# Kernel tuning notes

Measured on AMD Instinct MI355X. Metric: run time of the kernel, lower is better.

Reference implementation:

```python
import jax, jax.numpy as jnp
import numpy as np

# 3D multi-scale deformable attention (MSDeformAttn, n_heads=8 / 3D variant)
LEVEL_SHAPES = [(32, 32, 32), (16, 16, 16), (8, 8, 8), (4, 4, 4)]  # (H, W, D) per level
D_MODEL, N_HEADS, N_LEVELS, N_POINTS = 256, 8, 4, 4
C_HEAD = D_MODEL // N_HEADS  # 32
N_BATCH, LEN_Q = 1, 37440
LEN_IN = sum(h * w * d for h, w, d in LEVEL_SHAPES)  # 37440


def setup_inputs() -> dict:
    key = jax.random.key(0)
    ks = jax.random.split(key, 10)
    s = 0.02  # param init scale
    return {
        "query": jax.random.normal(ks[0], (N_BATCH, LEN_Q, D_MODEL), jnp.float32),
        "reference_points": jax.random.uniform(ks[1], (N_BATCH, LEN_Q, N_LEVELS, 3), jnp.float32),
        "input_flatten": jax.random.normal(ks[2], (N_BATCH, LEN_IN, D_MODEL), jnp.float32),
        "input_spatial_shapes": jnp.array(LEVEL_SHAPES, dtype=jnp.int32),
        "input_level_start_index": jnp.array(
            np.cumsum([0] + [h * w * d for h, w, d in LEVEL_SHAPES])[:-1], dtype=jnp.int32),
        "W_value": s * jax.random.normal(ks[3], (D_MODEL, D_MODEL), jnp.float32),
        "b_value": jnp.zeros((D_MODEL,), jnp.float32),
        "W_off": s * jax.random.normal(ks[4], (D_MODEL, N_HEADS * N_LEVELS * N_POINTS * 3), jnp.float32),
        "b_off": s * jax.random.normal(ks[5], (N_HEADS * N_LEVELS * N_POINTS * 3,), jnp.float32),
        "W_attn": s * jax.random.normal(ks[6], (D_MODEL, N_HEADS * N_LEVELS * N_POINTS), jnp.float32),
        "b_attn": jnp.zeros((N_HEADS * N_LEVELS * N_POINTS,), jnp.float32),
        "W_out": s * jax.random.normal(ks[7], (D_MODEL, D_MODEL), jnp.float32),
        "b_out": jnp.zeros((D_MODEL,), jnp.float32),
    }


def trilinear_sample(vol, gx, gy, gz):
    """torch F.grid_sample 3D, mode=bilinear, padding=zeros, align_corners=False.
    vol: (B, C, Dz, Dy, Dx); gx indexes Dx, gy indexes Dy, gz indexes Dz, each (B, Q) in [-1,1].
    Returns (B, C, Q)."""
    B, C, Dz, Dy, Dx = vol.shape
    ix = ((gx + 1.0) * Dx - 1.0) * 0.5
    iy = ((gy + 1.0) * Dy - 1.0) * 0.5
    iz = ((gz + 1.0) * Dz - 1.0) * 0.5
    x0f, y0f, z0f = jnp.floor(ix), jnp.floor(iy), jnp.floor(iz)
    fx, fy, fz = ix - x0f, iy - y0f, iz - z0f
    x0, y0, z0 = x0f.astype(jnp.int32), y0f.astype(jnp.int32), z0f.astype(jnp.int32)
    vol_f = vol.reshape(B, C, Dz * Dy * Dx)
    out = jnp.zeros((B, C, gx.shape[1]), vol.dtype)
    for dz in (0, 1):
        for dy in (0, 1):
            for dx in (0, 1):
                xc, yc, zc = x0 + dx, y0 + dy, z0 + dz
                w = ((fx if dx else 1.0 - fx) * (fy if dy else 1.0 - fy) * (fz if dz else 1.0 - fz))
                valid = ((xc >= 0) & (xc < Dx) & (yc >= 0) & (yc < Dy) & (zc >= 0) & (zc < Dz))
                idx = (jnp.clip(zc, 0, Dz - 1) * Dy + jnp.clip(yc, 0, Dy - 1)) * Dx + jnp.clip(xc, 0, Dx - 1)
                v = jnp.take_along_axis(vol_f, idx[:, None, :], axis=2)  # (B, C, Q)
                out = out + (w * valid.astype(w.dtype))[:, None, :] * v
    return out


def reference(query, reference_points, input_flatten, input_spatial_shapes,
              input_level_start_index, W_value, b_value, W_off, b_off,
              W_attn, b_attn, W_out, b_out):
    N, Lq, _ = query.shape
    Lin = input_flatten.shape[1]
    value = (input_flatten @ W_value + b_value).reshape(N, Lin, N_HEADS, C_HEAD)
    off = (query @ W_off + b_off).reshape(N, Lq, N_HEADS, N_LEVELS, N_POINTS, 3)
    attn = jax.nn.softmax((query @ W_attn + b_attn).reshape(N, Lq, N_HEADS, N_LEVELS * N_POINTS), axis=-1)
    # offset_normalizer = [W, H, D] per level (as in the torch code)
    norm = jnp.stack([input_spatial_shapes[:, 1], input_spatial_shapes[:, 0],
                      input_spatial_shapes[:, 2]], -1).astype(query.dtype)
    loc = reference_points[:, :, None, :, None, :] + off / norm[None, None, None, :, None, :]
    grids = 2.0 * loc - 1.0  # (N, Lq, M, L, P, 3)
    starts = np.cumsum([0] + [h * w * d for h, w, d in LEVEL_SHAPES])
    sampled = []
    for l, (H, W, D) in enumerate(LEVEL_SHAPES):
        vl = value[:, starts[l]:starts[l + 1]]  # (N, H*W*D, M, C)
        vol = (vl.reshape(N, H, W, D, N_HEADS, C_HEAD)
                 .transpose(0, 4, 5, 1, 2, 3)
                 .reshape(N * N_HEADS, C_HEAD, H, W, D))
        g = grids[:, :, :, l].transpose(0, 2, 1, 3, 4).reshape(N * N_HEADS, Lq * N_POINTS, 3)
        # grid x indexes last vol dim (D), y indexes W, z indexes H (torch grid_sample convention)
        s = trilinear_sample(vol, g[..., 0], g[..., 1], g[..., 2])  # (N*M, C, Lq*P)
        sampled.append(s.reshape(N * N_HEADS, C_HEAD, Lq, N_POINTS))
    samp = jnp.stack(sampled, axis=-2).reshape(N * N_HEADS, C_HEAD, Lq, N_LEVELS * N_POINTS)
    aw = attn.transpose(0, 2, 1, 3).reshape(N * N_HEADS, 1, Lq, N_LEVELS * N_POINTS)
    out = (samp * aw).sum(-1).reshape(N, N_HEADS * C_HEAD, Lq).transpose(0, 2, 1)
    return out @ W_out + b_out
```

## Files before the change

### kernel.cpp

```cpp
#include <hip/hip_runtime.h>
#include <math.h>

#define LQ      37440
#define LIN     37440
#define DMODEL  256
#define NHEADS  8
#define CHEAD   32
#define K_DIM   256

#define VALB_DELTA (LIN * 256 + 32)

typedef __attribute__((ext_vector_type(8))) short short8;
typedef __attribute__((ext_vector_type(4))) short short4v;
typedef __attribute__((ext_vector_type(4))) float f32x4;
typedef __attribute__((ext_vector_type(2))) float f32x2;

__device__ inline unsigned short bf16_rte(float f) {
    union { float f; unsigned u; } v; v.f = f;
    return (unsigned short)((v.u + 0x7fffu + ((v.u >> 16) & 1u)) >> 16);
}
__device__ inline float bf16_f(unsigned short s) {
    union { unsigned u; float f; } v; v.u = ((unsigned)s) << 16;
    return v.f;
}
__device__ inline float bits_f(unsigned u) {
    union { unsigned u; float f; } v; v.u = u;
    return v.f;
}
__device__ inline unsigned pkbf(float a, float b) {
    return (unsigned)bf16_rte(a) | ((unsigned)bf16_rte(b) << 16);
}

__device__ __forceinline__ void gl_lds16(const unsigned short* g, unsigned short* l) {
    __builtin_amdgcn_global_load_lds(
        (const __attribute__((address_space(1))) void*)g,
        (__attribute__((address_space(3))) void*)l, 16, 0, 0);
}

__global__ __launch_bounds__(256) void prep_all(
        const float* __restrict__ inp, const float* __restrict__ query,
        const float* __restrict__ Wv, const float* __restrict__ Wo,
        const float* __restrict__ Wa, const float* __restrict__ Wout,
        const float* __restrict__ bo, const float* __restrict__ ba,
        unsigned short* __restrict__ in_b, unsigned short* __restrict__ q_b,
        unsigned short* __restrict__ Bv, unsigned short* __restrict__ Bq,
        unsigned short* __restrict__ Bw, float* __restrict__ bias_m,
        unsigned short* __restrict__ padA,
        unsigned short* __restrict__ valB,
        int n4)
{
    const int bid = blockIdx.x;
    if (bid < 9360) {
        int i = bid * 256 + threadIdx.x;
        int j = i * 2;
        const float* src;
        unsigned short* dst;
        int jj;
        if (j < n4) { src = inp;   dst = in_b; jj = j; }
        else        { src = query; dst = q_b;  jj = j - n4; }
        float4 v0 = ((const float4*)src)[jj];
        float4 v1 = ((const float4*)src)[jj + 1];
        int4 o;
        o.x = (int)pkbf(v0.x, v0.y);
        o.y = (int)pkbf(v0.z, v0.w);
        o.z = (int)pkbf(v1.x, v1.y);
        o.w = (int)pkbf(v1.z, v1.w);
        ((int4*)dst)[jj >> 1] = o;
    } else {
        int i = (bid - 9360) * 256 + threadIdx.x;
        int n = i >> 8, k = i & 255;
        if (n < 256) {
            Bv[(size_t)n * 256 + k] = bf16_rte(Wv[(size_t)k * 256 + n]);
        } else if (n < 640) {
            int m = n - 256;
            Bq[(size_t)m * 256 + k] = bf16_rte(Wo[(size_t)k * 384 + m]);
        } else if (n < 768) {
            int m = n - 640;
            Bq[(size_t)(384 + m) * 256 + k] = bf16_rte(Wa[(size_t)k * 128 + m]);
        } else {
            int m = n - 768;
            Bw[(size_t)m * 256 + k] = bf16_rte(Wout[(size_t)k * 256 + m]);
        }
        if (i < 512) bias_m[i] = (i < 384) ? bo[i] : ba[i - 384];
        if (i < 64)       padA[i] = 0;
        else if (i < 96)  valB[i - 64] = 0;
        else if (i < 192) valB[(size_t)LIN * 256 + 32 + (i - 96)] = 0;
    }
}

__global__ __launch_bounds__(256) void gemm2(
    const unsigned short* __restrict__ in_b, const unsigned short* __restrict__ q_b,
    const unsigned short* __restrict__ Bv,   const unsigned short* __restrict__ Bq,
    const float* __restrict__ bv, const float* __restrict__ bias_m,
    unsigned short* __restrict__ value_t, unsigned short* __restrict__ valB,
    unsigned short* __restrict__ qbuf)
{
    __shared__ __align__(16) unsigned short SH[16384];
    unsigned short* AsL = SH;
    unsigned short* BsL = SH + 8192;

    const int t    = threadIdx.x;
    const int bm   = blockIdx.y * 128;
    const int w    = t >> 6;
    const int lane = t & 63;
    const int lm   = lane & 15;
    const int quad = lane >> 4;

    const int isval = (blockIdx.x < 2);
    const unsigned short* A  = isval ? in_b : q_b;
    const unsigned short* Bt = isval ? Bv : Bq;
    const float* bias        = isval ? bv : bias_m;
    const int n0             = (isval ? blockIdx.x : (blockIdx.x - 2)) * 128;

    const unsigned short* ga[2]; const unsigned short* gb[2];
    int loff[2];
    #pragma unroll
    for (int i = 0; i < 2; ++i) {
        int idx = i * 256 + t;
        int row = idx >> 2;
        int chn = (idx & 3) ^ ((row >> 1) & 3);
        int rga = bm + row; if (rga >= LQ) rga = LQ - 1;
        ga[i] = A  + (size_t)rga * K_DIM + chn * 8;
        gb[i] = Bt + (size_t)(n0 + row) * K_DIM + chn * 8;
        loff[i] = i * 2048 + w * 512;
    }

    const int ra0 = w * 32 + lm, ra1 = ra0 + 16;
    const int aoff0 = ra0 * 32 + ((quad ^ ((ra0 >> 1) & 3)) << 3);
    const int aoff1 = ra1 * 32 + ((quad ^ ((ra1 >> 1) & 3)) << 3);
    int boff[8];
    #pragma unroll
    for (int nt = 0; nt < 8; ++nt) {
        int rb = nt * 16 + lm;
        boff[nt] = rb * 32 + ((quad ^ ((rb >> 1) & 3)) << 3);
    }

    f32x4 acc[2][8];
    #pragma unroll
    for (int mt = 0; mt < 2; ++mt)
        #pragma unroll
        for (int nt = 0; nt < 8; ++nt)
            acc[mt][nt] = (f32x4){0.f, 0.f, 0.f, 0.f};

    #define STAGE(K0, SEL) do { \
        gl_lds16(ga[0] + (K0), AsL + (SEL) * 4096 + loff[0]); \
        gl_lds16(ga[1] + (K0), AsL + (SEL) * 4096 + loff[1]); \
        gl_lds16(gb[0] + (K0), BsL + (SEL) * 4096 + loff[0]); \
        gl_lds16(gb[1] + (K0), BsL + (SEL) * 4096 + loff[1]); \
    } while (0)

    STAGE(0, 0);
    #pragma unroll
    for (int kt = 0; kt < 8; ++kt) {
        const int sel = kt & 1;
        if (kt < 7) {
            STAGE((kt + 1) * 32, sel ^ 1);
            asm volatile("s_waitcnt vmcnt(4)" ::: "memory");
        } else {
            asm volatile("s_waitcnt vmcnt(0)" ::: "memory");
        }
        __builtin_amdgcn_s_barrier();

        const int so = sel * 4096;
        short8 af[2], bf[8];
        af[0] = *(const short8*)&AsL[so + aoff0];
        af[1] = *(const short8*)&AsL[so + aoff1];
        #pragma unroll
        for (int nt = 0; nt < 8; ++nt)
            bf[nt] = *(const short8*)&BsL[so + boff[nt]];
        #pragma unroll
        for (int mt = 0; mt < 2; ++mt)
            #pragma unroll
            for (int nt = 0; nt < 8; ++nt)
                acc[mt][nt] = __builtin_amdgcn_mfma_f32_16x16x32_bf16(af[mt], bf[nt], acc[mt][nt], 0, 0, 0);

        asm volatile("s_waitcnt lgkmcnt(0)" ::: "memory");
        __builtin_amdgcn_s_barrier();
    }
    #undef STAGE

    unsigned short* SHc = SH;
    #pragma unroll
    for (int nt = 0; nt < 8; ++nt) {
        int col = nt * 16 + lm;
        float bb = bias[n0 + col];
        #pragma unroll
        for (int mt = 0; mt < 2; ++mt) {
            int rb = w * 32 + mt * 16 + quad * 4;
            #pragma unroll
            for (int r = 0; r < 4; ++r)
                SHc[(rb + r) * 128 + col] = bf16_rte(acc[mt][nt][r] + bb);
        }
    }
    __syncthreads();

    if (isval) {
        const int h0 = n0 >> 5;
        #pragma unroll
        for (int k = 0; k < 8; ++k) {
            int ci  = t + k * 256;
            int hl  = ci >> 9;
            int rem = ci & 511;
            int row = rem >> 2;
            int cq  = (rem & 3) << 3;
            int4 v = *(const int4*)&SHc[row * 128 + hl * 32 + cq];
            int grow = bm + row;
            if (grow < LQ) {
                size_t e = ((size_t)(h0 + hl) * LIN + grow) * 32 + cq;
                *(int4*)&value_t[e] = v;
                *(int4*)&valB[32 + e] = v;
            }
        }
    } else {
        #pragma unroll
        for (int k = 0; k < 8; ++k) {
            int ci  = t + k * 256;
            int row = ci >> 4;
            int cq  = (ci & 15) << 3;
            int4 v = *(const int4*)&SHc[row * 128 + cq];
            int grow = bm + row;
            if (grow < LQ)
                *(int4*)&qbuf[(size_t)grow * 512 + n0 + cq] = v;
        }
    }
}

__global__ __launch_bounds__(256) void gemm_out(
    const unsigned short* __restrict__ A, const unsigned short* __restrict__ Bt,
    const float* __restrict__ bias, float* __restrict__ Cout)
{
    __shared__ __align__(16) unsigned short SH[16384];
    unsigned short* AsL = SH;
    unsigned short* BsL = SH + 8192;

    const int t    = threadIdx.x;
    const int bm   = blockIdx.y * 128;
    const int n0   = blockIdx.x * 128;
    const int w    = t >> 6;
    const int lane = t & 63;
    const int lm   = lane & 15;
    const int quad = lane >> 4;

    const unsigned short* ga[2]; const unsigned short* gb[2];
    int loff[2];
    #pragma unroll
    for (int i = 0; i < 2; ++i) {
        int idx = i * 256 + t;
        int row = idx >> 2;
        int chn = (idx & 3) ^ ((row >> 1) & 3);
        int rga = bm + row; if (rga >= LQ) rga = LQ - 1;
        ga[i] = A  + (size_t)rga * K_DIM + chn * 8;
        gb[i] = Bt + (size_t)(n0 + row) * K_DIM + chn * 8;
        loff[i] = i * 2048 + w * 512;
    }

    const int ra0 = w * 32 + lm, ra1 = ra0 + 16;
    const int aoff0 = ra0 * 32 + ((quad ^ ((ra0 >> 1) & 3)) << 3);
    const int aoff1 = ra1 * 32 + ((quad ^ ((ra1 >> 1) & 3)) << 3);
    int boff[8];
    #pragma unroll
    for (int nt = 0; nt < 8; ++nt) {
        int rb = nt * 16 + lm;
        boff[nt] = rb * 32 + ((quad ^ ((rb >> 1) & 3)) << 3);
    }

    f32x4 acc[2][8];
    #pragma unroll
    for (int mt = 0; mt < 2; ++mt)
        #pragma unroll
        for (int nt = 0; nt < 8; ++nt)
            acc[mt][nt] = (f32x4){0.f, 0.f, 0.f, 0.f};

    #define STAGE(K0, SEL) do { \
        gl_lds16(ga[0] + (K0), AsL + (SEL) * 4096 + loff[0]); \
        gl_lds16(ga[1] + (K0), AsL + (SEL) * 4096 + loff[1]); \
        gl_lds16(gb[0] + (K0), BsL + (SEL) * 4096 + loff[0]); \
        gl_lds16(gb[1] + (K0), BsL + (SEL) * 4096 + loff[1]); \
    } while (0)

    STAGE(0, 0);
    #pragma unroll
    for (int kt = 0; kt < 8; ++kt) {
        const int sel = kt & 1;
        if (kt < 7) {
            STAGE((kt + 1) * 32, sel ^ 1);
            asm volatile("s_waitcnt vmcnt(4)" ::: "memory");
        } else {
            asm volatile("s_waitcnt vmcnt(0)" ::: "memory");
        }
        __builtin_amdgcn_s_barrier();

        const int so = sel * 4096;
        short8 af[2], bf[8];
        af[0] = *(const short8*)&AsL[so + aoff0];
        af[1] = *(const short8*)&AsL[so + aoff1];
        #pragma unroll
        for (int nt = 0; nt < 8; ++nt)
            bf[nt] = *(const short8*)&BsL[so + boff[nt]];
        #pragma unroll
        for (int mt = 0; mt < 2; ++mt)
            #pragma unroll
            for (int nt = 0; nt < 8; ++nt)
                acc[mt][nt] = __builtin_amdgcn_mfma_f32_16x16x32_bf16(af[mt], bf[nt], acc[mt][nt], 0, 0, 0);

        asm volatile("s_waitcnt lgkmcnt(0)" ::: "memory");
        __builtin_amdgcn_s_barrier();
    }
    #undef STAGE

    float* SHf = (float*)SH;
    #pragma unroll
    for (int p = 0; p < 2; ++p) {
        if (p) __syncthreads();
        #pragma unroll
        for (int nt = 0; nt < 8; ++nt) {
            int col = nt * 16 + lm;
            float bb = bias[n0 + col];
            int lrow = w * 16 + quad * 4;
            #pragma unroll
            for (int r = 0; r < 4; ++r)
                SHf[(lrow + r) * 128 + col] = acc[p][nt][r] + bb;
        }
        __syncthreads();
        #pragma unroll
        for (int k = 0; k < 8; ++k) {
            int ci  = t + k * 256;
            int lr  = ci >> 5;
            int cq  = (ci & 31) << 2;
            int4 v = *(const int4*)&SHf[lr * 128 + cq];
            int grow = bm + (lr >> 4) * 32 + p * 16 + (lr & 15);
            if (grow < LQ)
                *(int4*)&Cout[(size_t)grow * 256 + n0 + cq] = v;
        }
    }
}

__global__ __launch_bounds__(256) void sample_kernel(
    const float* __restrict__ refp,
    const unsigned short* __restrict__ qbuf,
    const unsigned short* __restrict__ value_t,
    unsigned short* __restrict__ samp)
{
    __shared__ float4 zywS[4][16][8];
    __shared__ f32x2  wxS [4][16][8];
    __shared__ int4   ozyS[4][16][8];

    const int t  = threadIdx.x;
    const int q0 = blockIdx.x * 4;

    const int   Sz[4]   = {32, 16, 8, 4};
    const float invS[4] = {1.f/32.f, 1.f/16.f, 1.f/8.f, 1.f/4.f};
    const int   St[4]   = {0, 32768, 36864, 37376};

    #pragma unroll
    for (int pi = t; pi < 512; pi += 256) {
        int ql = pi >> 7;
        int hp = pi & 127;
        int hh = hp >> 4;
        int c  = hp & 15;
        int l  = c >> 2;
        int q  = q0 + ql;
        const unsigned short* o = qbuf + (size_t)q * 512 + hp * 3;
        const float* r = refp + q * 12 + l * 3;
        const int   S  = Sz[l];
        const float Sf = (float)S;
        const float is = invS[l];
        float ix = (r[0] + bf16_f(o[0]) * is) * Sf - 0.5f;
        float iy = (r[1] + bf16_f(o[1]) * is) * Sf - 0.5f;
        float iz = (r[2] + bf16_f(o[2]) * is) * Sf - 0.5f;
        float xf = floorf(ix), yf = floorf(iy), zf = floorf(iz);
        float fx = ix - xf, fy = iy - yf, fz = iz - zf;
        int x0 = (int)xf, y0 = (int)yf, z0 = (int)zf;

        float wx0 = (x0 >= 0  && x0 < S)     ? (1.f - fx) : 0.f;
        float wx1 = (x0 >= -1 && x0 < S - 1) ? fx         : 0.f;
        float wy0 = (y0 >= 0  && y0 < S)     ? (1.f - fy) : 0.f;
        float wy1 = (y0 >= -1 && y0 < S - 1) ? fy         : 0.f;
        float wz0 = (z0 >= 0  && z0 < S)     ? (1.f - fz) : 0.f;
        float wz1 = (z0 >= -1 && z0 < S - 1) ? fz         : 0.f;

        int cy0 = min(max(y0, 0), S - 1), cy1 = min(max(y0 + 1, 0), S - 1);
        int cz0 = min(max(z0, 0), S - 1), cz1 = min(max(z0 + 1, 0), S - 1);

        float lgv = bf16_f(qbuf[(size_t)q * 512 + 384 + hp]);
        float m = fmaxf(lgv, __shfl_xor(lgv, 1));
        m = fmaxf(m, __shfl_xor(m, 2));
        m = fmaxf(m, __shfl_xor(m, 4));
        m = fmaxf(m, __shfl_xor(m, 8));
        float e = __expf(lgv - m);
        float s = e + __shfl_xor(e, 1);
        s += __shfl_xor(s, 2);
        s += __shfl_xor(s, 4);
        s += __shfl_xor(s, 8);
        float a = __fdividef(e, s);

        const int S2 = S * S;
        const int st = St[l];
        const int xb = x0 * 32 + ((x0 & 1) ? VALB_DELTA : 0);
        zywS[ql][c][hh] = make_float4(wz0*wy0, wz0*wy1, wz1*wy0, wz1*wy1);
        wxS [ql][c][hh] = (f32x2){wx0 * a, wx1 * a};
        ozyS[ql][c][hh] = make_int4((st + cz0*S2 + cy0*S) * 32 + xb,
                                    (st + cz0*S2 + cy1*S) * 32 + xb,
                                    (st + cz1*S2 + cy0*S) * 32 + xb,
                                    (st + cz1*S2 + cy1*S) * 32 + xb);
    }
    __syncthreads();

    const int ql   = t >> 6;
    const int lane = t & 63;
    const int hh   = lane >> 3;
    const int j    = lane & 7;
    const int xsel = j >> 2;
    const int cgrp = (j & 3) << 3;
    const int q    = q0 + ql;

    const unsigned short* vbase = value_t - 64;
    const unsigned laneoff = (unsigned)(hh * (LIN * 32) + j * 8 + 64);

    f32x2 acc0 = {0.f,0.f}, acc1 = {0.f,0.f}, acc2 = {0.f,0.f}, acc3 = {0.f,0.f};

    #pragma unroll
    for (int c = 0; c < 16; ++c) {
        float4 zyw = zywS[ql][c][hh];
        f32x2  wx  = wxS [ql][c][hh];
        int4   zo  = ozyS[ql][c][hh];
        float  ws  = xsel ? wx.y : wx.x;

        #define CORNER(OFF, WZ) { \
            int4 v = *(const int4*)(vbase + (laneoff + (unsigned)(OFF))); \
            float w_ = (WZ) * ws; \
            f32x2 w2 = {w_, w_}; \
            acc0 += w2 * (f32x2){bits_f(((unsigned)v.x) << 16), bits_f((unsigned)v.x)}; \
            acc1 += w2 * (f32x2){bits_f(((unsigned)v.y) << 16), bits_f((unsigned)v.y)}; \
            acc2 += w2 * (f32x2){bits_f(((unsigned)v.z) << 16), bits_f((unsigned)v.z)}; \
            acc3 += w2 * (f32x2){bits_f(((unsigned)v.w) << 16), bits_f((unsigned)v.w)}; }

        CORNER(zo.x, zyw.x);
        CORNER(zo.y, zyw.y);
        CORNER(zo.z, zyw.z);
        CORNER(zo.w, zyw.w);
        #undef CORNER
    }

    float c0 = acc0.x + __shfl_xor(acc0.x, 4);
    float c1 = acc0.y + __shfl_xor(acc0.y, 4);
    float c2 = acc1.x + __shfl_xor(acc1.x, 4);
    float c3 = acc1.y + __shfl_xor(acc1.y, 4);
    float c4 = acc2.x + __shfl_xor(acc2.x, 4);
    float c5 = acc2.y + __shfl_xor(acc2.y, 4);
    float c6 = acc3.x + __shfl_xor(acc3.x, 4);
    float c7 = acc3.y + __shfl_xor(acc3.y, 4);
    if (xsel == 0) {
        int4 o = make_int4((int)pkbf(c0, c1), (int)pkbf(c2, c3),
                           (int)pkbf(c4, c5), (int)pkbf(c6, c7));
        *(int4*)(samp + (size_t)q * DMODEL + hh * CHEAD + cgrp) = o;
    }
}

extern "C" void kernel_launch(void* const* d_in, const int* in_sizes, int n_in,
                              void* d_out, int out_size, void* d_ws, size_t ws_size,
                              hipStream_t stream) {
    const float* query = (const float*)d_in[0];
    const float* refp  = (const float*)d_in[1];
    const float* inp   = (const float*)d_in[2];
    const float* Wv   = (const float*)d_in[5];
    const float* bv   = (const float*)d_in[6];
    const float* Wo   = (const float*)d_in[7];
    const float* bo   = (const float*)d_in[8];
    const float* Wa   = (const float*)d_in[9];
    const float* ba   = (const float*)d_in[10];
    const float* Wout = (const float*)d_in[11];
    const float* bout = (const float*)d_in[12];

    char* p = (char*)d_ws;
    p += 256;
    unsigned short* value_t = (unsigned short*)p; p += (size_t)LIN * 256 * 2;
    unsigned short* valB    = (unsigned short*)p; p += ((size_t)LIN * 256 + 128) * 2;
    unsigned short* qbuf    = (unsigned short*)p; p += (size_t)LQ * 512 * 2;
    unsigned short* samp    = (unsigned short*)p; p += (size_t)LQ * 256 * 2;
    unsigned short* in_b    = (unsigned short*)p; p += (size_t)LQ * 256 * 2;
    unsigned short* q_b     = (unsigned short*)p; p += (size_t)LQ * 256 * 2;
    unsigned short* Bv   = (unsigned short*)p;    p += 256 * 256 * 2;
    unsigned short* Bq   = (unsigned short*)p;    p += 512 * 256 * 2;
    unsigned short* Bw   = (unsigned short*)p;    p += 256 * 256 * 2;
    float* bias_m = (float*)p;                    p += 512 * 4;

    const int n4 = LQ * 256 / 4;
    dim3 blk(256);

    prep_all<<<9360 + 1024, blk, 0, stream>>>(
        inp, query, Wv, Wo, Wa, Wout, bo, ba,
        in_b, q_b, Bv, Bq, Bw, bias_m, value_t - 64, valB, n4);
    gemm2<<<dim3(6, (LQ + 127) / 128), blk, 0, stream>>>(
        in_b, q_b, Bv, Bq, bv, bias_m, value_t, valB, qbuf);
    sample_kernel<<<LQ / 4, blk, 0, stream>>>(refp, qbuf, value_t, samp);
    gemm_out<<<dim3(2, (LQ + 127) / 128), blk, 0, stream>>>(samp, Bw, bout, (float*)d_out);
}
```

Measured before the change: 295.1 us.

## Fuse fp32-to-bf16 activation conversion into GEMM and remap blocks per XCD

The separate conversion pass that turned input and query into bf16 buffers is removed. The GEMM now loads the fp32 A rows directly, converts them in registers and writes them into the swizzled LDS tile, overlapping that work with the MFMA loop. This saves one full write and re-read of two 37440x256 activation tensors. Both GEMMs also remap block IDs so that consecutive tiles stay on the same XCD for L2 locality, and the sampling kernel is split into two half-range launches. The trade-offs are twice the A-operand global bytes inside the GEMM, a full vmcnt(0) wait each iteration instead of the earlier partial wait, and one extra kernel launch.

```diff
diff --git a/kernel.cpp b/kernel.cpp
--- a/kernel.cpp
+++ b/kernel.cpp
@@ -37,59 +37,37 @@
         (__attribute__((address_space(3))) void*)l, 16, 0, 0);
 }
 
-__global__ __launch_bounds__(256) void prep_all(
-        const float* __restrict__ inp, const float* __restrict__ query,
+__global__ __launch_bounds__(256) void prep_w(
         const float* __restrict__ Wv, const float* __restrict__ Wo,
         const float* __restrict__ Wa, const float* __restrict__ Wout,
         const float* __restrict__ bo, const float* __restrict__ ba,
-        unsigned short* __restrict__ in_b, unsigned short* __restrict__ q_b,
         unsigned short* __restrict__ Bv, unsigned short* __restrict__ Bq,
         unsigned short* __restrict__ Bw, float* __restrict__ bias_m,
         unsigned short* __restrict__ padA,
-        unsigned short* __restrict__ valB,
-        int n4)
+        unsigned short* __restrict__ valB)
 {
-    const int bid = blockIdx.x;
-    if (bid < 9360) {
-        int i = bid * 256 + threadIdx.x;
-        int j = i * 2;
-        const float* src;
-        unsigned short* dst;
-        int jj;
-        if (j < n4) { src = inp;   dst = in_b; jj = j; }
-        else        { src = query; dst = q_b;  jj = j - n4; }
-        float4 v0 = ((const float4*)src)[jj];
-        float4 v1 = ((const float4*)src)[jj + 1];
-        int4 o;
-        o.x = (int)pkbf(v0.x, v0.y);
-        o.y = (int)pkbf(v0.z, v0.w);
-        o.z = (int)pkbf(v1.x, v1.y);
-        o.w = (int)pkbf(v1.z, v1.w);
-        ((int4*)dst)[jj >> 1] = o;
+    int i = blockIdx.x * 256 + threadIdx.x;
+    int n = i >> 8, k = i & 255;
+    if (n < 256) {
+        Bv[(size_t)n * 256 + k] = bf16_rte(Wv[(size_t)k * 256 + n]);
+    } else if (n < 640) {
+        int m = n - 256;
+        Bq[(size_t)m * 256 + k] = bf16_rte(Wo[(size_t)k * 384 + m]);
+    } else if (n < 768) {
+        int m = n - 640;
+        Bq[(size_t)(384 + m) * 256 + k] = bf16_rte(Wa[(size_t)k * 128 + m]);
     } else {
-        int i = (bid - 9360) * 256 + threadIdx.x;
-        int n = i >> 8, k = i & 255;
-        if (n < 256) {
-            Bv[(size_t)n * 256 + k] = bf16_rte(Wv[(size_t)k * 256 + n]);
-        } else if (n < 640) {
-            int m = n - 256;
-            Bq[(size_t)m * 256 + k] = bf16_rte(Wo[(size_t)k * 384 + m]);
-        } else if (n < 768) {
-            int m = n - 640;
-            Bq[(size_t)(384 + m) * 256 + k] = bf16_rte(Wa[(size_t)k * 128 + m]);
-        } else {
-            int m = n - 768;
-            Bw[(size_t)m * 256 + k] = bf16_rte(Wout[(size_t)k * 256 + m]);
-        }
-        if (i < 512) bias_m[i] = (i < 384) ? bo[i] : ba[i - 384];
-        if (i < 64)       padA[i] = 0;
-        else if (i < 96)  valB[i - 64] = 0;
-        else if (i < 192) valB[(size_t)LIN * 256 + 32 + (i - 96)] = 0;
-    }
+        int m = n - 768;
+        Bw[(size_t)m * 256 + k] = bf16_rte(Wout[(size_t)k * 256 + m]);
+    }
+    if (i < 512) bias_m[i] = (i < 384) ? bo[i] : ba[i - 384];
+    if (i < 64)       padA[i] = 0;
+    else if (i < 96)  valB[i - 64] = 0;
+    else if (i < 192) valB[(size_t)LIN * 256 + 32 + (i - 96)] = 0;
 }
 
 __global__ __launch_bounds__(256) void gemm2(
-    const unsigned short* __restrict__ in_b, const unsigned short* __restrict__ q_b,
+    const float* __restrict__ inp, const float* __restrict__ query,
     const unsigned short* __restrict__ Bv,   const unsigned short* __restrict__ Bq,
     const float* __restrict__ bv, const float* __restrict__ bias_m,
     unsigned short* __restrict__ value_t, unsigned short* __restrict__ valB,
@@ -100,30 +78,41 @@
     unsigned short* BsL = SH + 8192;
 
     const int t    = threadIdx.x;
-    const int bm   = blockIdx.y * 128;
     const int w    = t >> 6;
     const int lane = t & 63;
     const int lm   = lane & 15;
     const int quad = lane >> 4;
 
-    const int isval = (blockIdx.x < 2);
-    const unsigned short* A  = isval ? in_b : q_b;
+    const int g   = blockIdx.y * 6 + blockIdx.x;
+    const int xcd = g & 7, idx = g >> 3;
+    const int wg  = (xcd < 6 ? xcd * 220 : 1320 + (xcd - 6) * 219) + idx;
+    const int bx  = wg % 6;
+    const int by  = wg / 6;
+    const int bm  = by * 128;
+
+    const int isval = (bx < 2);
+    const float* Afp         = isval ? inp : query;
     const unsigned short* Bt = isval ? Bv : Bq;
     const float* bias        = isval ? bv : bias_m;
-    const int n0             = (isval ? blockIdx.x : (blockIdx.x - 2)) * 128;
-
-    const unsigned short* ga[2]; const unsigned short* gb[2];
-    int loff[2];
+    const int n0             = (isval ? bx : (bx - 2)) * 128;
+
+    const unsigned short* gb[2]; int loffB[2];
     #pragma unroll
     for (int i = 0; i < 2; ++i) {
-        int idx = i * 256 + t;
-        int row = idx >> 2;
-        int chn = (idx & 3) ^ ((row >> 1) & 3);
-        int rga = bm + row; if (rga >= LQ) rga = LQ - 1;
-        ga[i] = A  + (size_t)rga * K_DIM + chn * 8;
+        int idx2 = i * 256 + t;
+        int row = idx2 >> 2;
+        int chn = (idx2 & 3) ^ ((row >> 1) & 3);
         gb[i] = Bt + (size_t)(n0 + row) * K_DIM + chn * 8;
-        loff[i] = i * 2048 + w * 512;
-    }
+        loffB[i] = i * 2048 + w * 512;
+    }
+
+    const int aRow = t >> 1;
+    const int aK   = (t & 1) * 16;
+    int rga = bm + aRow; if (rga >= LQ) rga = LQ - 1;
+    const float* gA = Afp + (size_t)rga * K_DIM + aK;
+    const int aSwz  = (aRow >> 1) & 3;
+    const int aSlot0 = aRow * 32 + (((((t & 1) << 1))     ^ aSwz) << 3);
+    const int aSlot1 = aRow * 32 + (((((t & 1) << 1) + 1) ^ aSwz) << 3);
 
     const int ra0 = w * 32 + lm, ra1 = ra0 + 16;
     const int aoff0 = ra0 * 32 + ((quad ^ ((ra0 >> 1) & 3)) << 3);
@@ -142,24 +131,34 @@
         for (int nt = 0; nt < 8; ++nt)
             acc[mt][nt] = (f32x4){0.f, 0.f, 0.f, 0.f};
 
-    #define STAGE(K0, SEL) do { \
-        gl_lds16(ga[0] + (K0), AsL + (SEL) * 4096 + loff[0]); \
-        gl_lds16(ga[1] + (K0), AsL + (SEL) * 4096 + loff[1]); \
-        gl_lds16(gb[0] + (K0), BsL + (SEL) * 4096 + loff[0]); \
-        gl_lds16(gb[1] + (K0), BsL + (SEL) * 4096 + loff[1]); \
-    } while (0)
-
-    STAGE(0, 0);
+    float4 f0, f1, f2, f3;
+    #define LOADA(K0) do { const float4* pA_ = (const float4*)(gA + (K0)); \
+        f0 = pA_[0]; f1 = pA_[1]; f2 = pA_[2]; f3 = pA_[3]; } while (0)
+    #define GLB(K0, SEL) do { \
+        gl_lds16(gb[0] + (K0), BsL + (SEL) * 4096 + loffB[0]); \
+        gl_lds16(gb[1] + (K0), BsL + (SEL) * 4096 + loffB[1]); } while (0)
+    #define CVTA(SEL) do { \
+        unsigned short* bufp_ = AsL + (SEL) * 4096; \
+        int4 wlo_ = make_int4((int)pkbf(f0.x,f0.y), (int)pkbf(f0.z,f0.w), \
+                              (int)pkbf(f1.x,f1.y), (int)pkbf(f1.z,f1.w)); \
+        int4 whi_ = make_int4((int)pkbf(f2.x,f2.y), (int)pkbf(f2.z,f2.w), \
+                              (int)pkbf(f3.x,f3.y), (int)pkbf(f3.z,f3.w)); \
+        *(int4*)&bufp_[aSlot0] = wlo_; \
+        *(int4*)&bufp_[aSlot1] = whi_; } while (0)
+
+    LOADA(0);
+    GLB(0, 0);
+    CVTA(0);
+    asm volatile("s_waitcnt vmcnt(0) lgkmcnt(0)" ::: "memory");
+    __builtin_amdgcn_s_barrier();
+
     #pragma unroll
     for (int kt = 0; kt < 8; ++kt) {
         const int sel = kt & 1;
         if (kt < 7) {
-            STAGE((kt + 1) * 32, sel ^ 1);
-            asm volatile("s_waitcnt vmcnt(4)" ::: "memory");
-        } else {
-            asm volatile("s_waitcnt vmcnt(0)" ::: "memory");
-        }
-        __builtin_amdgcn_s_barrier();
+            LOADA((kt + 1) * 32);
+            GLB((kt + 1) * 32, sel ^ 1);
+        }
 
         const int so = sel * 4096;
         short8 af[2], bf[8];
@@ -174,10 +173,14 @@
             for (int nt = 0; nt < 8; ++nt)
                 acc[mt][nt] = __builtin_amdgcn_mfma_f32_16x16x32_bf16(af[mt], bf[nt], acc[mt][nt], 0, 0, 0);
 
-        asm volatile("s_waitcnt lgkmcnt(0)" ::: "memory");
+        if (kt < 7) CVTA(sel ^ 1);
+
+        asm volatile("s_waitcnt vmcnt(0) lgkmcnt(0)" ::: "memory");
         __builtin_amdgcn_s_barrier();
     }
-    #undef STAGE
+    #undef LOADA
+    #undef GLB
+    #undef CVTA
 
     unsigned short* SHc = SH;
     #pragma unroll
@@ -234,20 +237,24 @@
     unsigned short* BsL = SH + 8192;
 
     const int t    = threadIdx.x;
-    const int bm   = blockIdx.y * 128;
-    const int n0   = blockIdx.x * 128;
     const int w    = t >> 6;
     const int lane = t & 63;
     const int lm   = lane & 15;
     const int quad = lane >> 4;
 
+    const int g   = blockIdx.y * 2 + blockIdx.x;
+    const int xcd = g & 7, idx = g >> 3;
+    const int wg  = (xcd < 2 ? xcd * 74 : 148 + (xcd - 2) * 73) + idx;
+    const int n0  = (wg % 2) * 128;
+    const int bm  = (wg / 2) * 128;
+
     const unsigned short* ga[2]; const unsigned short* gb[2];
     int loff[2];
     #pragma unroll
     for (int i = 0; i < 2; ++i) {
-        int idx = i * 256 + t;
-        int row = idx >> 2;
-        int chn = (idx & 3) ^ ((row >> 1) & 3);
+        int idx2 = i * 256 + t;
+        int row = idx2 >> 2;
+        int chn = (idx2 & 3) ^ ((row >> 1) & 3);
         int rga = bm + row; if (rga >= LQ) rga = LQ - 1;
         ga[i] = A  + (size_t)rga * K_DIM + chn * 8;
         gb[i] = Bt + (size_t)(n0 + row) * K_DIM + chn * 8;
@@ -339,14 +346,15 @@
     const float* __restrict__ refp,
     const unsigned short* __restrict__ qbuf,
     const unsigned short* __restrict__ value_t,
-    unsigned short* __restrict__ samp)
+    unsigned short* __restrict__ samp,
+    int qbase)
 {
     __shared__ float4 zywS[4][16][8];
     __shared__ f32x2  wxS [4][16][8];
     __shared__ int4   ozyS[4][16][8];
 
     const int t  = threadIdx.x;
-    const int q0 = blockIdx.x * 4;
+    const int q0 = qbase + blockIdx.x * 4;
 
     const int   Sz[4]   = {32, 16, 8, 4};
     const float invS[4] = {1.f/32.f, 1.f/16.f, 1.f/8.f, 1.f/4.f};
@@ -478,21 +486,18 @@
     unsigned short* valB    = (unsigned short*)p; p += ((size_t)LIN * 256 + 128) * 2;
     unsigned short* qbuf    = (unsigned short*)p; p += (size_t)LQ * 512 * 2;
     unsigned short* samp    = (unsigned short*)p; p += (size_t)LQ * 256 * 2;
-    unsigned short* in_b    = (unsigned short*)p; p += (size_t)LQ * 256 * 2;
-    unsigned short* q_b     = (unsigned short*)p; p += (size_t)LQ * 256 * 2;
     unsigned short* Bv   = (unsigned short*)p;    p += 256 * 256 * 2;
     unsigned short* Bq   = (unsigned short*)p;    p += 512 * 256 * 2;
     unsigned short* Bw   = (unsigned short*)p;    p += 256 * 256 * 2;
     float* bias_m = (float*)p;                    p += 512 * 4;
 
-    const int n4 = LQ * 256 / 4;
     dim3 blk(256);
 
-    prep_all<<<9360 + 1024, blk, 0, stream>>>(
-        inp, query, Wv, Wo, Wa, Wout, bo, ba,
-        in_b, q_b, Bv, Bq, Bw, bias_m, value_t - 64, valB, n4);
+    prep_w<<<1024, blk, 0, stream>>>(
+        Wv, Wo, Wa, Wout, bo, ba, Bv, Bq, Bw, bias_m, value_t - 64, valB);
     gemm2<<<dim3(6, (LQ + 127) / 128), blk, 0, stream>>>(
-        in_b, q_b, Bv, Bq, bv, bias_m, value_t, valB, qbuf);
-    sample_kernel<<<LQ / 4, blk, 0, stream>>>(refp, qbuf, value_t, samp);
+        inp, query, Bv, Bq, bv, bias_m, value_t, valB, qbuf);
+    sample_kernel<<<LQ / 8, blk, 0, stream>>>(refp, qbuf, value_t, samp, 0);
+    sample_kernel<<<LQ / 8, blk, 0, stream>>>(refp, qbuf, value_t, samp, LQ / 2);
     gemm_out<<<dim3(2, (LQ + 127) / 128), blk, 0, stream>>>(samp, Bw, bout, (float*)d_out);
 }
```

Result: slower. 318.9 us (+8.1%).
